# Performance work log

Hardware: AMD Instinct MI355X
Metric: run time of the kernel (lower is better)

The kernel has to match this reference:

```python
import jax, jax.numpy as jnp
import numpy as np

B, S = 256, 512
V, E, H, O = 32000, 1024, 1024, 512


def setup_inputs() -> dict:
    key = jax.random.key(0)
    ks = jax.random.split(key, 8)
    s = 1.0 / np.sqrt(H)
    return {
        "x": jax.random.randint(ks[0], (B, S), 0, V),
        "emb": jax.random.normal(ks[1], (V, E), jnp.float32) * 0.02,
        "W_ih": jax.random.normal(ks[2], (H, E), jnp.float32) * s,
        "b_ih": jax.random.normal(ks[3], (H,), jnp.float32) * s,
        "W_hh": jax.random.normal(ks[4], (H, H), jnp.float32) * s,
        "b_hh": jax.random.normal(ks[5], (H,), jnp.float32) * s,
        "W_clf": jax.random.normal(ks[6], (O, H), jnp.float32) * s,
        "b_clf": jax.random.normal(ks[7], (O,), jnp.float32) * s,
    }


def reference(x, emb, W_ih, b_ih, W_hh, b_hh, W_clf, b_clf):
    # Embedding lookup: [B, S, E]
    xe = emb[x]
    # Precompute input projections for all timesteps in one big GEMM:
    # [B, S, H] = einsum over E; this is mathematically identical to per-step x_t @ W_ih^T.
    xp = jnp.einsum("bse,he->bsh", xe, W_ih) + b_ih
    h0 = jnp.zeros((x.shape[0], W_hh.shape[0]), dtype=xe.dtype)

    def step(h, xp_t):
        h = jnp.tanh(xp_t + h @ W_hh.T + b_hh)
        return h, None

    # scan over time (leading axis): xp -> [S, B, H]
    h_final, _ = jax.lax.scan(step, h0, jnp.swapaxes(xp, 0, 1))
    # Final classifier on last hidden state (fc/dropout are unused in the original forward)
    return h_final @ W_clf.T + b_clf
```

## Files before the change

kernel.cpp:

```cpp
#include <hip/hip_runtime.h>
#include <hip/hip_bf16.h>

#define B_ 256
#define S_ 512
#define V_ 32000
#define E_ 1024
#define H_ 1024
#define O_ 512

typedef __hip_bfloat16 bf16;
typedef _Float16 f16;
typedef unsigned long long u64;
typedef __attribute__((ext_vector_type(8))) short bf16x8;
typedef __attribute__((ext_vector_type(8))) _Float16 f16x8;
typedef __attribute__((ext_vector_type(8))) float f32x8;
typedef __attribute__((ext_vector_type(4))) float f32x4;
typedef __attribute__((ext_vector_type(4))) int i32x4;

__device__ __forceinline__ f32x4 mfma_bf(bf16x8 a, bf16x8 b, f32x4 c) {
  return __builtin_amdgcn_mfma_f32_16x16x32_bf16(a, b, c, 0, 0, 0);
}
__device__ __forceinline__ f32x4 mfma_h(f16x8 a, f16x8 b, f32x4 c) {
  return __builtin_amdgcn_mfma_f32_16x16x32_f16(a, b, c, 0, 0, 0);
}

#if defined(__has_builtin)
#if __has_builtin(__builtin_amdgcn_global_load_lds)
#define HAS_GLL 1
#endif
#endif
#ifndef HAS_GLL
#define HAS_GLL 0
#endif

#define OFF_H     ((size_t)0)
#define OFF_CNT   ((size_t)1048576)
#define OFF_WHHHI ((size_t)1081344)
#define OFF_WHHLO ((size_t)3178496)
#define OFF_WIH   ((size_t)5275648)
#define OFF_WCLF  ((size_t)7372800)
#define OFF_EMB   ((size_t)8421376)
#define WS_MIN    ((size_t)8421376)
#define WS_FULL   ((size_t)73957376)

__global__ void init_zero_kernel(i32x4* __restrict__ p, int n4) {
  int i = blockIdx.x * 256 + threadIdx.x;
  if (i < n4) p[i] = (i32x4){0, 0, 0, 0};
}

__global__ void k_split_bf16(const float* __restrict__ s, bf16* __restrict__ hi,
                             bf16* __restrict__ lo, int n) {
  int i = blockIdx.x * 256 + threadIdx.x;
  if (i < n) {
    float v = s[i];
    bf16 h = __float2bfloat16(v);
    hi[i] = h;
    lo[i] = __float2bfloat16(v - __bfloat162float(h));
  }
}

__global__ void k_cvt_f16(const float* __restrict__ s, f16* __restrict__ d, int n) {
  int i = blockIdx.x * 256 + threadIdx.x;
  if (i < n) d[i] = (f16)s[i];
}

__global__ void k_cvt_bf16(const float* __restrict__ s, bf16* __restrict__ d, int n) {
  int i = blockIdx.x * 256 + threadIdx.x;
  if (i < n) d[i] = __float2bfloat16(s[i]);
}

__global__ __launch_bounds__(256, 1) void rnn_scan(
    const int* __restrict__ x,
    const float* __restrict__ emb_f32,
    const f16* __restrict__ emb_h,
    const int use_f16_emb,
    const f16* __restrict__ wih_h,
    const float* __restrict__ bih, const float* __restrict__ bhh,
    const bf16* __restrict__ whh_hi_g,
    const bf16* __restrict__ whh_lo_g,
    bf16* __restrict__ hbuf,
    int* __restrict__ cnt) {
  __shared__ short Wl[32 * 1024];
  __shared__ f32x4 redA[128];
  __shared__ f32x4 redB[128];

  const int tid = threadIdx.x, lane = tid & 63;
  const int w = tid >> 6, wm = w & 1, kh = w >> 1;
  const int gi = blockIdx.x & 7, gj = blockIdx.x >> 3;
  const int m0 = gi * 32, n0 = gj * 32;
  const int am = lane & 15, akc = lane >> 4;

  for (int q = tid; q < 32 * 128; q += 256) {
    int rr = q >> 7, c = q & 127;
    *(bf16x8*)&Wl[rr * 1024 + (c ^ (rr & 7)) * 8] =
        *(const bf16x8*)&whh_hi_g[(size_t)(n0 + rr) * H_ + c * 8];
  }

  bf16x8 wlo[2][16];
  f16x8 wih[2][16];
  float bsum[2];
  int nl[2];
#pragma unroll
  for (int ct = 0; ct < 2; ++ct) {
    const int n = n0 + ct * 16 + am;
    nl[ct] = ct * 16 + am;
    bsum[ct] = bih[n] + bhh[n];
#pragma unroll
    for (int kc = 0; kc < 16; ++kc) {
      const int k = kh * 512 + kc * 32 + akc * 8;
      wlo[ct][kc] = *(const bf16x8*)&whh_lo_g[(size_t)n * H_ + k];
      wih[ct][kc] = *(const f16x8*)&wih_h[(size_t)n * E_ + k];
    }
  }
  __syncthreads();

  const int arow = m0 + wm * 16 + am;
  const int koff = kh * 512 + akc * 8;
  const int mG = m0 + wm * 16 + (lane >> 4) * 4;
  const int myct = kh;
  const int nGm = n0 + myct * 16 + am;

  union cvt8 { u64 q[2]; bf16x8 v; };

  for (int t = 0; t < S_; ++t) {
    f32x4 a0a = {0.f,0.f,0.f,0.f}, a0b = {0.f,0.f,0.f,0.f};
    f32x4 a1a = {0.f,0.f,0.f,0.f}, a1b = {0.f,0.f,0.f,0.f};

    const int idx = x[arow * S_ + t];
    if (use_f16_emb) {
      const f16* er = emb_h + (size_t)idx * E_ + koff;
#pragma unroll
      for (int kc = 0; kc < 16; ++kc) {
        f16x8 a = *(const f16x8*)(er + kc * 32);
        a0a = mfma_h(a, wih[0][kc], a0a);
        a1a = mfma_h(a, wih[1][kc], a1a);
      }
    } else {
      const float* er = emb_f32 + (size_t)idx * E_ + koff;
#pragma unroll
      for (int kc = 0; kc < 16; ++kc) {
        f32x8 v = *(const f32x8*)(er + kc * 32);
        f16x8 a = __builtin_convertvector(v, f16x8);
        a0a = mfma_h(a, wih[0][kc], a0a);
        a1a = mfma_h(a, wih[1][kc], a1a);
      }
    }

    if (t > 0) {
      while (__hip_atomic_load(&cnt[t * 8 + gi], __ATOMIC_RELAXED,
                               __HIP_MEMORY_SCOPE_AGENT) < 32)
        __builtin_amdgcn_s_sleep(1);
      __builtin_amdgcn_fence(__ATOMIC_ACQUIRE, "workgroup");
    }

    const u64* hsrc = (const u64*)(hbuf + (size_t)(t & 1) * (B_ * H_) +
                                   (size_t)arow * H_ + koff);
    u64 hb[32];
#pragma unroll
    for (int kc = 0; kc < 16; ++kc) {
      hb[2 * kc]     = __hip_atomic_load(hsrc + kc * 8, __ATOMIC_RELAXED,
                                         __HIP_MEMORY_SCOPE_AGENT);
      hb[2 * kc + 1] = __hip_atomic_load(hsrc + kc * 8 + 1, __ATOMIC_RELAXED,
                                         __HIP_MEMORY_SCOPE_AGENT);
    }

#pragma unroll
    for (int kc = 0; kc < 16; ++kc) {
      cvt8 c;
      c.q[0] = hb[2 * kc];
      c.q[1] = hb[2 * kc + 1];
      bf16x8 a = c.v;
      const int cidx = kh * 64 + kc * 4 + akc;
      bf16x8 b0 = *(const bf16x8*)&Wl[nl[0] * 1024 + (cidx ^ (nl[0] & 7)) * 8];
      bf16x8 b1 = *(const bf16x8*)&Wl[nl[1] * 1024 + (cidx ^ (nl[1] & 7)) * 8];
      a0a = mfma_bf(a, b0, a0a);
      a0b = mfma_bf(a, wlo[0][kc], a0b);
      a1a = mfma_bf(a, b1, a1a);
      a1b = mfma_bf(a, wlo[1][kc], a1b);
    }

    f32x4 acc0 = a0a + a0b, acc1 = a1a + a1b;
    if (kh == 1) redA[tid & 127] = acc0; else redB[tid] = acc1;
    __syncthreads();
    f32x4 fin = (kh == 0) ? (acc0 + redA[tid]) : (acc1 + redB[tid & 127]);

    bf16* hdst = hbuf + (size_t)((t + 1) & 1) * (B_ * H_);
    const float bs = bsum[myct];
#pragma unroll
    for (int r = 0; r < 4; ++r) {
      bf16 hv = __float2bfloat16(tanhf(fin[r] + bs));
      __hip_atomic_store((unsigned short*)&hdst[(size_t)(mG + r) * H_ + nGm],
                         (unsigned short)__bfloat16_as_ushort(hv),
                         __ATOMIC_RELAXED, __HIP_MEMORY_SCOPE_AGENT);
    }

    __syncthreads();
    if (tid == 0)
      __hip_atomic_fetch_add(&cnt[(t + 1) * 8 + gi], 1, __ATOMIC_RELAXED,
                             __HIP_MEMORY_SCOPE_AGENT);
  }
}

__global__ __launch_bounds__(256, 2) void gemm_bias_kernel(
    const bf16* __restrict__ A, const bf16* __restrict__ Bw,
    const float* __restrict__ bias, float* __restrict__ Cc, int Ndim, int Kdim) {
  __shared__ bf16 At[128 * 64];
  __shared__ bf16 Bt[128 * 64];

  const int tid = threadIdx.x;
  const int wave = tid >> 6, lane = tid & 63;
  const int row0 = blockIdx.y * 128, col0 = blockIdx.x * 128;
  const int wm = wave & 1, wn = wave >> 1;

  f32x4 acc[4][4];
#pragma unroll
  for (int mi = 0; mi < 4; ++mi)
#pragma unroll
    for (int ni = 0; ni < 4; ++ni) acc[mi][ni] = (f32x4){0.f, 0.f, 0.f, 0.f};

  for (int kb = 0; kb < Kdim; kb += 64) {
#pragma unroll
    for (int it = 0; it < 4; ++it) {
      int q = it * 256 + tid;
      int rr = q >> 3, qc = (q & 7) * 8;
      const bf16* ga = A + (size_t)(row0 + rr) * Kdim + kb + qc;
      const bf16* gb = Bw + (size_t)(col0 + rr) * Kdim + kb + qc;
#if HAS_GLL
      __builtin_amdgcn_global_load_lds(
          (const __attribute__((address_space(1))) void*)ga,
          (__attribute__((address_space(3))) void*)((char*)At + (it * 4 + wave) * 1024),
          16, 0, 0);
      __builtin_amdgcn_global_load_lds(
          (const __attribute__((address_space(1))) void*)gb,
          (__attribute__((address_space(3))) void*)((char*)Bt + (it * 4 + wave) * 1024),
          16, 0, 0);
#else
      *(i32x4*)((char*)At + q * 16) = *(const i32x4*)ga;
      *(i32x4*)((char*)Bt + q * 16) = *(const i32x4*)gb;
#endif
    }
    __syncthreads();

#pragma unroll
    for (int ks = 0; ks < 2; ++ks) {
      const int ko = ks * 32 + (lane >> 4) * 8;
      bf16x8 af[4], bfr[4];
#pragma unroll
      for (int mi = 0; mi < 4; ++mi)
        af[mi] = *(const bf16x8*)&At[(wm * 64 + mi * 16 + (lane & 15)) * 64 + ko];
#pragma unroll
      for (int ni = 0; ni < 4; ++ni)
        bfr[ni] = *(const bf16x8*)&Bt[(wn * 64 + ni * 16 + (lane & 15)) * 64 + ko];
#pragma unroll
      for (int mi = 0; mi < 4; ++mi)
#pragma unroll
        for (int ni = 0; ni < 4; ++ni)
          acc[mi][ni] = mfma_bf(af[mi], bfr[ni], acc[mi][ni]);
    }
    __syncthreads();
  }

  const int crow = (lane >> 4) * 4, ccol = lane & 15;
#pragma unroll
  for (int ni = 0; ni < 4; ++ni) {
    const int gc = col0 + wn * 64 + ni * 16 + ccol;
    const float bv = bias[gc];
#pragma unroll
    for (int mi = 0; mi < 4; ++mi) {
      const int gr0 = row0 + wm * 64 + mi * 16 + crow;
#pragma unroll
      for (int r = 0; r < 4; ++r)
        Cc[(size_t)(gr0 + r) * Ndim + gc] = acc[mi][ni][r] + bv;
    }
  }
}

extern "C" void kernel_launch(void* const* d_in, const int* in_sizes, int n_in,
                              void* d_out, int out_size, void* d_ws, size_t ws_size,
                              hipStream_t stream) {
  const int*   x    = (const int*)d_in[0];
  const float* emb  = (const float*)d_in[1];
  const float* Wih  = (const float*)d_in[2];
  const float* bih  = (const float*)d_in[3];
  const float* Whh  = (const float*)d_in[4];
  const float* bhh  = (const float*)d_in[5];
  const float* Wclf = (const float*)d_in[6];
  const float* bclf = (const float*)d_in[7];
  float* out = (float*)d_out;

  char* ws = (char*)d_ws;
  bf16* hbuf   = (bf16*)(ws + OFF_H);
  int*  cnt    = (int*)(ws + OFF_CNT);
  bf16* whh_hi = (bf16*)(ws + OFF_WHHHI);
  bf16* whh_lo = (bf16*)(ws + OFF_WHHLO);
  f16*  wih_h  = (f16*)(ws + OFF_WIH);
  bf16* wclf_b = (bf16*)(ws + OFF_WCLF);
  f16*  emb_h  = (f16*)(ws + OFF_EMB);
  const int use_f16_emb = (ws_size >= WS_FULL) ? 1 : 0;

  init_zero_kernel<<<dim3(261), dim3(256), 0, stream>>>((i32x4*)ws, 66562);

  k_split_bf16<<<dim3(4096), dim3(256), 0, stream>>>(Whh, whh_hi, whh_lo, H_ * H_);
  k_cvt_f16<<<dim3(4096), dim3(256), 0, stream>>>(Wih, wih_h, H_ * E_);
  k_cvt_bf16<<<dim3(2048), dim3(256), 0, stream>>>(Wclf, wclf_b, O_ * H_);
  if (use_f16_emb)
    k_cvt_f16<<<dim3((V_ * E_ + 255) / 256), dim3(256), 0, stream>>>(emb, emb_h,
                                                                     V_ * E_);

  rnn_scan<<<dim3(256), dim3(256), 0, stream>>>(
      x, emb, emb_h, use_f16_emb, wih_h, bih, bhh, whh_hi, whh_lo, hbuf, cnt);

  gemm_bias_kernel<<<dim3(O_ / 128, B_ / 128), dim3(256), 0, stream>>>(
      hbuf, wclf_b, bclf, out, O_, H_);
}
```

Measured before the change: 4.542 ms.

## Replace atomic step counters with per-block flags and inline-asm coherent loads

Replaces the per-timestep atomic fetch_add counter with one flag word per producer block, which the block sets to the step number. A wave polls all 32 flags of its row group in a single load and checks them with a ballot. The hidden-state reads and writes become inline-asm global loads and stores with sc0 sc1 cache bypass. The 16 dwordx4 loads are issued back to back before a single wait, replacing the many 64-bit atomic loads, which should cut synchronisation and load latency on the serial scan. The risk is correctness: there are no acquire/release fences, so ordering rests on the explicit waits and the cache-bypass bits.

```diff
diff --git a/kernel.cpp b/kernel.cpp
--- a/kernel.cpp
+++ b/kernel.cpp
@@ -10,12 +10,13 @@
 
 typedef __hip_bfloat16 bf16;
 typedef _Float16 f16;
-typedef unsigned long long u64;
 typedef __attribute__((ext_vector_type(8))) short bf16x8;
 typedef __attribute__((ext_vector_type(8))) _Float16 f16x8;
 typedef __attribute__((ext_vector_type(8))) float f32x8;
 typedef __attribute__((ext_vector_type(4))) float f32x4;
 typedef __attribute__((ext_vector_type(4))) int i32x4;
+
+union icast { i32x4 i; bf16x8 h; };
 
 __device__ __forceinline__ f32x4 mfma_bf(bf16x8 a, bf16x8 b, f32x4 c) {
   return __builtin_amdgcn_mfma_f32_16x16x32_bf16(a, b, c, 0, 0, 0);
@@ -79,7 +80,7 @@
     const bf16* __restrict__ whh_hi_g,
     const bf16* __restrict__ whh_lo_g,
     bf16* __restrict__ hbuf,
-    int* __restrict__ cnt) {
+    int* __restrict__ flg) {
   __shared__ short Wl[32 * 1024];
   __shared__ f32x4 redA[128];
   __shared__ f32x4 redB[128];
@@ -99,11 +100,9 @@
   bf16x8 wlo[2][16];
   f16x8 wih[2][16];
   float bsum[2];
-  int nl[2];
 #pragma unroll
   for (int ct = 0; ct < 2; ++ct) {
     const int n = n0 + ct * 16 + am;
-    nl[ct] = ct * 16 + am;
     bsum[ct] = bih[n] + bhh[n];
 #pragma unroll
     for (int kc = 0; kc < 16; ++kc) {
@@ -114,13 +113,14 @@
   }
   __syncthreads();
 
+  const int nl0 = am, nl1 = 16 + am;
+  const int sw0 = nl0 & 7, sw1 = nl1 & 7;
   const int arow = m0 + wm * 16 + am;
   const int koff = kh * 512 + akc * 8;
   const int mG = m0 + wm * 16 + (lane >> 4) * 4;
-  const int myct = kh;
-  const int nGm = n0 + myct * 16 + am;
-
-  union cvt8 { u64 q[2]; bf16x8 v; };
+  const int nGm = n0 + kh * 16 + am;
+  const int* fp = flg + (gi << 5) + (lane & 31);
+  int* fpw = flg + (gi << 5) + gj;
 
   for (int t = 0; t < S_; ++t) {
     f32x4 a0a = {0.f,0.f,0.f,0.f}, a0b = {0.f,0.f,0.f,0.f};
@@ -147,37 +147,61 @@
     }
 
     if (t > 0) {
-      while (__hip_atomic_load(&cnt[t * 8 + gi], __ATOMIC_RELAXED,
-                               __HIP_MEMORY_SCOPE_AGENT) < 32)
+      int fv;
+      for (;;) {
+        asm volatile(
+            "global_load_dword %0, %1, off sc0 sc1\n\t"
+            "s_waitcnt vmcnt(0)"
+            : "=&v"(fv) : "v"(fp) : "memory");
+        if (__ballot(fv >= t) == ~0ull) break;
         __builtin_amdgcn_s_sleep(1);
-      __builtin_amdgcn_fence(__ATOMIC_ACQUIRE, "workgroup");
-    }
-
-    const u64* hsrc = (const u64*)(hbuf + (size_t)(t & 1) * (B_ * H_) +
-                                   (size_t)arow * H_ + koff);
-    u64 hb[32];
-#pragma unroll
-    for (int kc = 0; kc < 16; ++kc) {
-      hb[2 * kc]     = __hip_atomic_load(hsrc + kc * 8, __ATOMIC_RELAXED,
-                                         __HIP_MEMORY_SCOPE_AGENT);
-      hb[2 * kc + 1] = __hip_atomic_load(hsrc + kc * 8 + 1, __ATOMIC_RELAXED,
-                                         __HIP_MEMORY_SCOPE_AGENT);
-    }
-
-#pragma unroll
-    for (int kc = 0; kc < 16; ++kc) {
-      cvt8 c;
-      c.q[0] = hb[2 * kc];
-      c.q[1] = hb[2 * kc + 1];
-      bf16x8 a = c.v;
-      const int cidx = kh * 64 + kc * 4 + akc;
-      bf16x8 b0 = *(const bf16x8*)&Wl[nl[0] * 1024 + (cidx ^ (nl[0] & 7)) * 8];
-      bf16x8 b1 = *(const bf16x8*)&Wl[nl[1] * 1024 + (cidx ^ (nl[1] & 7)) * 8];
-      a0a = mfma_bf(a, b0, a0a);
-      a0b = mfma_bf(a, wlo[0][kc], a0b);
-      a1a = mfma_bf(a, b1, a1a);
-      a1b = mfma_bf(a, wlo[1][kc], a1b);
-    }
+      }
+    }
+
+    const bf16* hsrc = hbuf + (size_t)(t & 1) * (B_ * H_) +
+                       (size_t)arow * H_ + koff;
+    i32x4 q0,q1,q2,q3,q4,q5,q6,q7,q8,q9,q10,q11,q12,q13,q14,q15;
+    asm volatile(
+        "global_load_dwordx4 %0, %16, off sc0 sc1\n\t"
+        "global_load_dwordx4 %1, %16, off offset:64 sc0 sc1\n\t"
+        "global_load_dwordx4 %2, %16, off offset:128 sc0 sc1\n\t"
+        "global_load_dwordx4 %3, %16, off offset:192 sc0 sc1\n\t"
+        "global_load_dwordx4 %4, %16, off offset:256 sc0 sc1\n\t"
+        "global_load_dwordx4 %5, %16, off offset:320 sc0 sc1\n\t"
+        "global_load_dwordx4 %6, %16, off offset:384 sc0 sc1\n\t"
+        "global_load_dwordx4 %7, %16, off offset:448 sc0 sc1\n\t"
+        "global_load_dwordx4 %8, %16, off offset:512 sc0 sc1\n\t"
+        "global_load_dwordx4 %9, %16, off offset:576 sc0 sc1\n\t"
+        "global_load_dwordx4 %10, %16, off offset:640 sc0 sc1\n\t"
+        "global_load_dwordx4 %11, %16, off offset:704 sc0 sc1\n\t"
+        "global_load_dwordx4 %12, %16, off offset:768 sc0 sc1\n\t"
+        "global_load_dwordx4 %13, %16, off offset:832 sc0 sc1\n\t"
+        "global_load_dwordx4 %14, %16, off offset:896 sc0 sc1\n\t"
+        "global_load_dwordx4 %15, %16, off offset:960 sc0 sc1\n\t"
+        "s_waitcnt vmcnt(0)"
+        : "=&v"(q0), "=&v"(q1), "=&v"(q2), "=&v"(q3), "=&v"(q4), "=&v"(q5),
+          "=&v"(q6), "=&v"(q7), "=&v"(q8), "=&v"(q9), "=&v"(q10), "=&v"(q11),
+          "=&v"(q12), "=&v"(q13), "=&v"(q14), "=&v"(q15)
+        : "v"(hsrc)
+        : "memory");
+
+#define RSTEP(KC, QQ)                                                     \
+    {                                                                     \
+      icast _c; _c.i = (QQ);                                              \
+      bf16x8 a = _c.h;                                                    \
+      const int cidx = kh * 64 + (KC) * 4 + akc;                          \
+      bf16x8 b0 = *(const bf16x8*)&Wl[nl0 * 1024 + (cidx ^ sw0) * 8];     \
+      bf16x8 b1 = *(const bf16x8*)&Wl[nl1 * 1024 + (cidx ^ sw1) * 8];     \
+      a0a = mfma_bf(a, b0, a0a);                                          \
+      a0b = mfma_bf(a, wlo[0][KC], a0b);                                  \
+      a1a = mfma_bf(a, b1, a1a);                                          \
+      a1b = mfma_bf(a, wlo[1][KC], a1b);                                  \
+    }
+    RSTEP(0, q0)   RSTEP(1, q1)   RSTEP(2, q2)   RSTEP(3, q3)
+    RSTEP(4, q4)   RSTEP(5, q5)   RSTEP(6, q6)   RSTEP(7, q7)
+    RSTEP(8, q8)   RSTEP(9, q9)   RSTEP(10, q10) RSTEP(11, q11)
+    RSTEP(12, q12) RSTEP(13, q13) RSTEP(14, q14) RSTEP(15, q15)
+#undef RSTEP
 
     f32x4 acc0 = a0a + a0b, acc1 = a1a + a1b;
     if (kh == 1) redA[tid & 127] = acc0; else redB[tid] = acc1;
@@ -185,19 +209,28 @@
     f32x4 fin = (kh == 0) ? (acc0 + redA[tid]) : (acc1 + redB[tid & 127]);
 
     bf16* hdst = hbuf + (size_t)((t + 1) & 1) * (B_ * H_);
-    const float bs = bsum[myct];
-#pragma unroll
-    for (int r = 0; r < 4; ++r) {
-      bf16 hv = __float2bfloat16(tanhf(fin[r] + bs));
-      __hip_atomic_store((unsigned short*)&hdst[(size_t)(mG + r) * H_ + nGm],
-                         (unsigned short)__bfloat16_as_ushort(hv),
-                         __ATOMIC_RELAXED, __HIP_MEMORY_SCOPE_AGENT);
-    }
+    const float bs = bsum[kh];
+    unsigned d0 = __bfloat16_as_ushort(__float2bfloat16(tanhf(fin[0] + bs)));
+    unsigned d1 = __bfloat16_as_ushort(__float2bfloat16(tanhf(fin[1] + bs)));
+    unsigned d2 = __bfloat16_as_ushort(__float2bfloat16(tanhf(fin[2] + bs)));
+    unsigned d3 = __bfloat16_as_ushort(__float2bfloat16(tanhf(fin[3] + bs)));
+    const bf16* sa0 = hdst + (size_t)mG * H_ + nGm;
+    const bf16* sa1 = sa0 + 2 * H_;
+    asm volatile(
+        "global_store_short %0, %2, off sc0 sc1\n\t"
+        "global_store_short %0, %3, off offset:2048 sc0 sc1\n\t"
+        "global_store_short %1, %4, off sc0 sc1\n\t"
+        "global_store_short %1, %5, off offset:2048 sc0 sc1\n\t"
+        "s_waitcnt vmcnt(0)"
+        :: "v"(sa0), "v"(sa1), "v"(d0), "v"(d1), "v"(d2), "v"(d3)
+        : "memory");
 
     __syncthreads();
-    if (tid == 0)
-      __hip_atomic_fetch_add(&cnt[(t + 1) * 8 + gi], 1, __ATOMIC_RELAXED,
-                             __HIP_MEMORY_SCOPE_AGENT);
+    if (tid == 0) {
+      int fo = t + 1;
+      asm volatile("global_store_dword %0, %1, off sc0 sc1"
+                   :: "v"(fpw), "v"(fo) : "memory");
+    }
   }
 }
 
@@ -290,7 +323,7 @@
 
   char* ws = (char*)d_ws;
   bf16* hbuf   = (bf16*)(ws + OFF_H);
-  int*  cnt    = (int*)(ws + OFF_CNT);
+  int*  flg    = (int*)(ws + OFF_CNT);
   bf16* whh_hi = (bf16*)(ws + OFF_WHHHI);
   bf16* whh_lo = (bf16*)(ws + OFF_WHHLO);
   f16*  wih_h  = (f16*)(ws + OFF_WIH);
@@ -308,7 +341,7 @@
                                                                      V_ * E_);
 
   rnn_scan<<<dim3(256), dim3(256), 0, stream>>>(
-      x, emb, emb_h, use_f16_emb, wih_h, bih, bhh, whh_hi, whh_lo, hbuf, cnt);
+      x, emb, emb_h, use_f16_emb, wih_h, bih, bhh, whh_hi, whh_lo, hbuf, flg);
 
   gemm_bias_kernel<<<dim3(O_ / 128, B_ / 128), dim3(256), 0, stream>>>(
       hbuf, wclf_b, bclf, out, O_, H_);
```

Result: faster. 4.408 ms (-3.0%).
